# Performance work log

Measured on AMD Instinct MI355X. Metric: run time of the kernel, lower is better.

## Reference

```python
import jax, jax.numpy as jnp
import numpy as np

D_MODEL = 256
NHEAD = 8
D_FF = 2 * D_MODEL
N_LAYERS = 4
LAYER_NAMES = ("self", "cross", "self", "cross")
EPS_ATTN = 1e-6
EPS_LN = 1e-5


def pos_encoding(x):
    # LoFTR-style 2D sinusoidal positional encoding, x: [N, C, H, W]
    n, c, h, w = x.shape
    d4 = c // 4
    # exp(arange(0, c//2, 2) * (-log(1e4) / (c//2)))
    div = jnp.exp(jnp.arange(d4, dtype=jnp.float32) * 2.0 * (-np.log(10000.0) / (c // 2)))
    xs = jnp.arange(w, dtype=jnp.float32)[None, None, :]   # [1,1,W]
    ys = jnp.arange(h, dtype=jnp.float32)[None, :, None]   # [1,H,1]
    dv = div[:, None, None]                                 # [d4,1,1]
    sx = jnp.broadcast_to(jnp.sin(xs * dv), (d4, h, w))
    cx = jnp.broadcast_to(jnp.cos(xs * dv), (d4, h, w))
    sy = jnp.broadcast_to(jnp.sin(ys * dv), (d4, h, w))
    cy = jnp.broadcast_to(jnp.cos(ys * dv), (d4, h, w))
    pe = jnp.stack([sx, cx, sy, cy], axis=1).reshape(c, h, w)  # channel order pe[0::4]=sin_x,...
    return x + pe[None]


def linear_attention(q, k, v):
    # q: [N,L,H,d], k/v: [N,S,H,d]
    Q = jax.nn.elu(q) + 1.0
    K = jax.nn.elu(k) + 1.0
    KV = jnp.einsum('nshd,nshm->nhmd', K, v)                 # [N,H,d,d]
    Z = 1.0 / (jnp.einsum('nlhd,nhd->nlh', Q, K.sum(axis=1)) + EPS_ATTN)
    return jnp.einsum('nlhd,nhmd,nlh->nlhm', Q, KV, Z)       # [N,L,H,d]


def layer_norm(x, g, b):
    m = jnp.mean(x, axis=-1, keepdims=True)
    v = jnp.mean(jnp.square(x - m), axis=-1, keepdims=True)
    return (x - m) / jnp.sqrt(v + EPS_LN) * g + b


def encoder_layer(x, src, p):
    N, L, _ = x.shape
    q = (x @ p['Wq'] + p['bq']).reshape(N, L, NHEAD, -1)
    S = src.shape[1]
    k = (src @ p['Wk'] + p['bk']).reshape(N, S, NHEAD, -1)
    v = (src @ p['Wv'] + p['bv']).reshape(N, S, NHEAD, -1)
    attn = linear_attention(q, k, v).reshape(N, L, -1) @ p['Wo'] + p['bo']
    x = layer_norm(x + attn, p['g1'], p['be1'])
    y = jax.nn.relu(x @ p['W1'] + p['b1']) @ p['W2'] + p['b2']
    return layer_norm(x + y, p['g2'], p['be2'])


def _params_at(i, Wq, bq, Wk, bk, Wv, bv, Wo, bo, W1, b1, W2, b2, g1, be1, g2, be2):
    return dict(Wq=Wq[i], bq=bq[i], Wk=Wk[i], bk=bk[i], Wv=Wv[i], bv=bv[i],
                Wo=Wo[i], bo=bo[i], W1=W1[i], b1=b1[i], W2=W2[i], b2=b2[i],
                g1=g1[i], be1=be1[i], g2=g2[i], be2=be2[i])


def setup_inputs() -> dict:
    key = jax.random.key(0)
    ks = jax.random.split(key, 16)
    N, C, H, W = 4, D_MODEL, 64, 64
    d, dff, Ln = D_MODEL, D_FF, N_LAYERS
    s = 1.0 / np.sqrt(d)
    sf = 1.0 / np.sqrt(dff)
    return {
        'ref_feature': jax.random.normal(ks[0], (N, C, H, W), jnp.float32),
        'src_feature': jax.random.normal(ks[1], (N, C, H, W), jnp.float32),
        'Wq': jax.random.normal(ks[2], (Ln, d, d), jnp.float32) * s,
        'bq': jnp.zeros((Ln, d), jnp.float32),
        'Wk': jax.random.normal(ks[3], (Ln, d, d), jnp.float32) * s,
        'bk': jnp.zeros((Ln, d), jnp.float32),
        'Wv': jax.random.normal(ks[4], (Ln, d, d), jnp.float32) * s,
        'bv': jnp.zeros((Ln, d), jnp.float32),
        'Wo': jax.random.normal(ks[5], (Ln, d, d), jnp.float32) * s,
        'bo': jnp.zeros((Ln, d), jnp.float32),
        'W1': jax.random.normal(ks[6], (Ln, d, dff), jnp.float32) * s,
        'b1': jnp.zeros((Ln, dff), jnp.float32),
        'W2': jax.random.normal(ks[7], (Ln, dff, d), jnp.float32) * sf,
        'b2': jnp.zeros((Ln, d), jnp.float32),
        'g1': jnp.ones((Ln, d), jnp.float32),
        'be1': jnp.zeros((Ln, d), jnp.float32),
        'g2': jnp.ones((Ln, d), jnp.float32),
        'be2': jnp.zeros((Ln, d), jnp.float32),
    }


def reference(ref_feature, src_feature, Wq, bq, Wk, bk, Wv, bv, Wo, bo,
              W1, b1, W2, b2, g1, be1, g2, be2):
    # FMT.forward(feat='cross')
    N, C, H, W = ref_feature.shape
    f0 = pos_encoding(ref_feature).transpose(0, 2, 3, 1).reshape(N, H * W, C)
    f1 = pos_encoding(src_feature).transpose(0, 2, 3, 1).reshape(N, H * W, C)
    p1 = jnp.concatenate([f0, f1], axis=0)   # [2N, L, C]
    p2 = jnp.concatenate([f1, f0], axis=0)
    for i, name in enumerate(LAYER_NAMES):
        p = _params_at(i, Wq, bq, Wk, bk, Wv, bv, Wo, bo, W1, b1, W2, b2, g1, be1, g2, be2)
        src = p1 if name == 'self' else p2
        p1 = encoder_layer(p1, src, p)
    out = p1.reshape(2 * N, H, W, C).transpose(0, 3, 1, 2)  # [2N, C, H, W]
    return out
```

## Files before the change

### kernel.cpp

```cpp
#include <hip/hip_runtime.h>
#include <hip/hip_bf16.h>

typedef __bf16 bf16;
typedef __attribute__((ext_vector_type(8))) __bf16 bf16x8;
typedef __attribute__((ext_vector_type(4))) __bf16 bf16x4;
typedef __attribute__((ext_vector_type(4))) float f32x4;

__device__ __forceinline__ bf16 f2bf(float f) { return (bf16)f; }

__device__ __forceinline__ void async_cp16(const void* g, void* l) {
    __builtin_amdgcn_global_load_lds(
        (const __attribute__((address_space(1))) unsigned int*)g,
        (__attribute__((address_space(3))) unsigned int*)l, 16, 0, 0);
}

__device__ __forceinline__ float pe_val(int c, int t) {
    int h = t >> 6, w = t & 63;
    int i = c >> 2, j = c & 3;
    float div = expf(-0.14391156831212787f * (float)i);
    float arg = ((j < 2) ? (float)w : (float)h) * div;
    return (j & 1) ? cosf(arg) : sinf(arg);
}

__global__ __launch_bounds__(1024) void encode_kernel(const float* __restrict__ ref,
                                                      const float* __restrict__ src,
                                                      bf16* __restrict__ Xb,
                                                      bf16* __restrict__ P2b) {
    __shared__ float tile[32][33];
    int n = blockIdx.z >> 1, sel = blockIdx.z & 1;
    const float* f = sel ? src : ref;
    int t = blockIdx.x * 32 + threadIdx.x;
    int c = blockIdx.y * 32 + threadIdx.y;
    float v = f[((size_t)n * 256 + c) * 4096 + t] + pe_val(c, t);
    tile[threadIdx.y][threadIdx.x] = v;
    __syncthreads();
    int tt = blockIdx.x * 32 + threadIdx.y;
    int cc = blockIdx.y * 32 + threadIdx.x;
    float o = tile[threadIdx.x][threadIdx.y];
    int bx = sel ? 4 + n : n;
    int bp = sel ? n : 4 + n;
    Xb [((size_t)bx * 4096 + tt) * 256 + cc] = f2bf(o);
    P2b[((size_t)bp * 4096 + tt) * 256 + cc] = f2bf(o);
}

__global__ __launch_bounds__(1024) void wt_conv(const float* __restrict__ Wq, const float* __restrict__ Wk,
                                                const float* __restrict__ Wv, const float* __restrict__ Wo,
                                                const float* __restrict__ W1, const float* __restrict__ W2,
                                                bf16* __restrict__ Wt) {
    __shared__ float t[32][33];
    int z = blockIdx.z, L = z / 6, m = z - L * 6;
    const float* src; int K, N, doff;
    if      (m == 0) { src = Wq + L * 65536;  K = 256; N = 256; doff = 0; }
    else if (m == 1) { src = Wk + L * 65536;  K = 256; N = 256; doff = 65536; }
    else if (m == 2) { src = Wv + L * 65536;  K = 256; N = 256; doff = 131072; }
    else if (m == 3) { src = Wo + L * 65536;  K = 256; N = 256; doff = 196608; }
    else if (m == 4) { src = W1 + L * 131072; K = 256; N = 512; doff = 262144; }
    else             { src = W2 + L * 131072; K = 512; N = 256; doff = 393216; }
    int n0 = blockIdx.x * 32, k0 = blockIdx.y * 32;
    if (n0 >= N || k0 >= K) return;
    t[threadIdx.y][threadIdx.x] = src[(size_t)(k0 + threadIdx.y) * N + n0 + threadIdx.x];
    __syncthreads();
    bf16* dst = Wt + (size_t)L * 524288 + doff;
    dst[(size_t)(n0 + threadIdx.y) * K + k0 + threadIdx.x] = f2bf(t[threadIdx.x][threadIdx.y]);
}

__global__ __launch_bounds__(256) void gemm_qkv(const bf16* __restrict__ Aq,
                                                const bf16* __restrict__ Akv,
                                                const bf16* __restrict__ Wt,
                                                const float* __restrict__ bq,
                                                const float* __restrict__ bk,
                                                const float* __restrict__ bv,
                                                bf16* __restrict__ Q,
                                                bf16* __restrict__ Ko,
                                                bf16* __restrict__ V) {
    __shared__ bf16 Als[128 * 64];
    __shared__ bf16 Bls[128 * 64];
    int tid = threadIdx.x;
    int wave = tid >> 6, lane = tid & 63;
    int bm = blockIdx.y * 128, bn = blockIdx.x * 128;
    int wm = (wave >> 1) * 64, wn = (wave & 1) * 64;
    int l15 = lane & 15, g = lane >> 4;
    const int K = 256;

    int seg = bn >> 8, cloc = bn & 255;
    const bf16* A = seg == 0 ? Aq : Akv;
    const float* bias = seg == 0 ? bq : (seg == 1 ? bk : bv);
    bf16* Out = seg == 0 ? Q : (seg == 1 ? Ko : V);
    bool do_elu = seg < 2;

    f32x4 acc[4][4] = {};

    for (int k0 = 0; k0 < K; k0 += 64) {
#pragma unroll
        for (int r = 0; r < 4; ++r) {
            int Lc = r * 256 + tid;
            int row = Lc >> 3, cs = Lc & 7;
            int gc = cs ^ (row & 7);
            async_cp16(A  + (size_t)(bm + row) * K + k0 + gc * 8, &Als[Lc * 8]);
            async_cp16(Wt + (size_t)(bn + row) * K + k0 + gc * 8, &Bls[Lc * 8]);
        }
        __syncthreads();
#pragma unroll
        for (int ks = 0; ks < 2; ++ks) {
            bf16x8 af[4], bfr[4];
#pragma unroll
            for (int i = 0; i < 4; ++i) {
                int row = wm + i * 16 + l15;
                int c = ks * 4 + g;
                af[i] = *(bf16x8*)&Als[row * 64 + ((c ^ (row & 7)) * 8)];
            }
#pragma unroll
            for (int j = 0; j < 4; ++j) {
                int row = wn + j * 16 + l15;
                int c = ks * 4 + g;
                bfr[j] = *(bf16x8*)&Bls[row * 64 + ((c ^ (row & 7)) * 8)];
            }
#pragma unroll
            for (int i = 0; i < 4; ++i)
#pragma unroll
                for (int j = 0; j < 4; ++j)
                    acc[i][j] = __builtin_amdgcn_mfma_f32_16x16x32_bf16(af[i], bfr[j], acc[i][j], 0, 0, 0);
        }
        __syncthreads();
    }

    int r4 = (lane >> 4) * 4;
#pragma unroll
    for (int i = 0; i < 4; ++i) {
#pragma unroll
        for (int j = 0; j < 4; ++j) {
            int cj = cloc + wn + j * 16 + l15;
            float bvv = bias[cj];
#pragma unroll
            for (int r = 0; r < 4; ++r) {
                int row = bm + wm + i * 16 + r4 + r;
                float v = acc[i][j][r] + bvv;
                if (do_elu) v = v > 0.f ? v + 1.f : expf(v);
                Out[(size_t)row * 256 + cj] = f2bf(v);
            }
        }
    }
}

template <int RELU>
__global__ __launch_bounds__(256) void gemm_mfma(const bf16* __restrict__ A,
                                                 const bf16* __restrict__ Wt,
                                                 const float* __restrict__ bias,
                                                 bf16* __restrict__ C,
                                                 int N, int K) {
    __shared__ bf16 Als[128 * 64];
    __shared__ bf16 Bls[128 * 64];
    int tid = threadIdx.x;
    int wave = tid >> 6, lane = tid & 63;
    int bm = blockIdx.y * 128, bn = blockIdx.x * 128;
    int wm = (wave >> 1) * 64, wn = (wave & 1) * 64;
    int l15 = lane & 15, g = lane >> 4;

    f32x4 acc[4][4] = {};

    for (int k0 = 0; k0 < K; k0 += 64) {
#pragma unroll
        for (int r = 0; r < 4; ++r) {
            int Lc = r * 256 + tid;
            int row = Lc >> 3, cs = Lc & 7;
            int gc = cs ^ (row & 7);
            async_cp16(A  + (size_t)(bm + row) * K + k0 + gc * 8, &Als[Lc * 8]);
            async_cp16(Wt + (size_t)(bn + row) * K + k0 + gc * 8, &Bls[Lc * 8]);
        }
        __syncthreads();
#pragma unroll
        for (int ks = 0; ks < 2; ++ks) {
            bf16x8 af[4], bfr[4];
#pragma unroll
            for (int i = 0; i < 4; ++i) {
                int row = wm + i * 16 + l15;
                int c = ks * 4 + g;
                af[i] = *(bf16x8*)&Als[row * 64 + ((c ^ (row & 7)) * 8)];
            }
#pragma unroll
            for (int j = 0; j < 4; ++j) {
                int row = wn + j * 16 + l15;
                int c = ks * 4 + g;
                bfr[j] = *(bf16x8*)&Bls[row * 64 + ((c ^ (row & 7)) * 8)];
            }
#pragma unroll
            for (int i = 0; i < 4; ++i)
#pragma unroll
                for (int j = 0; j < 4; ++j)
                    acc[i][j] = __builtin_amdgcn_mfma_f32_16x16x32_bf16(af[i], bfr[j], acc[i][j], 0, 0, 0);
        }
        __syncthreads();
    }

    int r4 = (lane >> 4) * 4;
#pragma unroll
    for (int i = 0; i < 4; ++i) {
#pragma unroll
        for (int j = 0; j < 4; ++j) {
            int col = bn + wn + j * 16 + l15;
            float bvv = bias[col];
#pragma unroll
            for (int r = 0; r < 4; ++r) {
                int row = bm + wm + i * 16 + r4 + r;
                float v = acc[i][j][r] + bvv;
                if (RELU) v = fmaxf(v, 0.f);
                C[(size_t)row * N + col] = f2bf(v);
            }
        }
    }
}

__global__ __launch_bounds__(256) void kv_prep_part(const bf16* __restrict__ Kb,
                                                    const bf16* __restrict__ Vb,
                                                    float* __restrict__ Pkv,
                                                    float* __restrict__ Pks) {
    __shared__ float Ks[128][32];
    __shared__ float Vs[128][32];
    int sp = blockIdx.x;
    int nh = blockIdx.y;
    int n = nh >> 3, h = nh & 7;
    int tid = threadIdx.x;
    int wave = tid >> 6, lane = tid & 63;
    int mg = lane >> 3;
    int dg = lane & 7;
    size_t base = ((size_t)n * 4096 + sp * 128) * 256 + h * 32;

#pragma unroll
    for (int p = 0; p < 2; ++p) {
        int r = p * 64 + (tid >> 2);
        int c = (tid & 3) * 8;
        bf16x8 k8 = *(const bf16x8*)(Kb + base + (size_t)r * 256 + c);
        bf16x8 v8 = *(const bf16x8*)(Vb + base + (size_t)r * 256 + c);
#pragma unroll
        for (int u = 0; u < 8; ++u) { Ks[r][c + u] = (float)k8[u]; Vs[r][c + u] = (float)v8[u]; }
    }
    __syncthreads();

    float acc[4][4] = {};
    float ks4[4] = {};
    int s0 = wave * 32;
    for (int s = s0; s < s0 + 32; ++s) {
        float4 kq = *(float4*)&Ks[s][dg * 4];
        float4 vq = *(float4*)&Vs[s][mg * 4];
        ks4[0] += kq.x; ks4[1] += kq.y; ks4[2] += kq.z; ks4[3] += kq.w;
        acc[0][0] += vq.x * kq.x; acc[0][1] += vq.x * kq.y; acc[0][2] += vq.x * kq.z; acc[0][3] += vq.x * kq.w;
        acc[1][0] += vq.y * kq.x; acc[1][1] += vq.y * kq.y; acc[1][2] += vq.y * kq.z; acc[1][3] += vq.y * kq.w;
        acc[2][0] += vq.z * kq.x; acc[2][1] += vq.z * kq.y; acc[2][2] += vq.z * kq.z; acc[2][3] += vq.z * kq.w;
        acc[3][0] += vq.w * kq.x; acc[3][1] += vq.w * kq.y; acc[3][2] += vq.w * kq.z; acc[3][3] += vq.w * kq.w;
    }
    __syncthreads();

    float* R  = &Ks[0][0];
    float* RS = &Vs[0][0];
#pragma unroll
    for (int mi = 0; mi < 4; ++mi)
#pragma unroll
        for (int dj = 0; dj < 4; ++dj)
            R[wave * 1024 + (mg * 4 + mi) * 32 + dg * 4 + dj] = acc[mi][dj];
    if (mg == 0)
#pragma unroll
        for (int dj = 0; dj < 4; ++dj) RS[wave * 32 + dg * 4 + dj] = ks4[dj];
    __syncthreads();

    int e = tid * 4;
    float4 o0 = *(float4*)&R[e];
    float4 o1 = *(float4*)&R[1024 + e];
    float4 o2 = *(float4*)&R[2048 + e];
    float4 o3 = *(float4*)&R[3072 + e];
    float4 o = make_float4(o0.x + o1.x + o2.x + o3.x, o0.y + o1.y + o2.y + o3.y,
                           o0.z + o1.z + o2.z + o3.z, o0.w + o1.w + o2.w + o3.w);
    *(float4*)&Pkv[((size_t)nh * 32 + sp) * 1024 + e] = o;
    if (tid < 32)
        Pks[((size_t)nh * 32 + sp) * 32 + tid] = RS[tid] + RS[32 + tid] + RS[64 + tid] + RS[96 + tid];
}

__global__ __launch_bounds__(256) void kv_reduce(const float* __restrict__ Pkv,
                                                 const float* __restrict__ Pks,
                                                 float* __restrict__ KV,
                                                 float* __restrict__ Ksum) {
    int nh = blockIdx.x;
    int e = threadIdx.x * 4;
    float4 s = make_float4(0.f, 0.f, 0.f, 0.f);
    for (int sp = 0; sp < 32; ++sp) {
        float4 p = *(const float4*)&Pkv[((size_t)nh * 32 + sp) * 1024 + e];
        s.x += p.x; s.y += p.y; s.z += p.z; s.w += p.w;
    }
    *(float4*)&KV[(size_t)nh * 1024 + e] = s;
    if (threadIdx.x < 32) {
        float ss = 0.f;
        for (int sp = 0; sp < 32; ++sp) ss += Pks[((size_t)nh * 32 + sp) * 32 + threadIdx.x];
        Ksum[nh * 32 + threadIdx.x] = ss;
    }
}

__global__ __launch_bounds__(256) void attn_apply(const bf16* __restrict__ Qb,
                                                  const float* __restrict__ KV,
                                                  const float* __restrict__ Ksum,
                                                  bf16* __restrict__ B) {
    __shared__ float Qs[32][260];
    __shared__ float Zs[32][8];
    int bx = blockIdx.x;
    int n = bx >> 7;
    int tok0 = (bx & 127) << 5;
    int tid = threadIdx.x;

    const bf16* qsrc = Qb + ((size_t)(n * 4096 + tok0)) * 256;
#pragma unroll
    for (int kk = 0; kk < 4; ++kk) {
        int e8 = tid + kk * 256;
        bf16x8 v = *(const bf16x8*)(qsrc + (size_t)e8 * 8);
        int t = e8 >> 5, c8 = e8 & 31;
#pragma unroll
        for (int u = 0; u < 8; ++u) Qs[t][c8 * 8 + u] = (float)v[u];
    }

    int h = tid >> 5, m = tid & 31;
    float kvr[32];
    const float* kvp = KV + (size_t)(n * 8 + h) * 1024 + m * 32;
#pragma unroll
    for (int c = 0; c < 8; ++c) *(float4*)&kvr[c * 4] = *(const float4*)(kvp + c * 4);
    __syncthreads();

    {
        int tz = tid >> 3, hz = tid & 7;
        const float* ksp = Ksum + n * 256 + hz * 32;
        float z = 0.f;
#pragma unroll
        for (int c = 0; c < 8; ++c) {
            float4 q = *(float4*)&Qs[tz][hz * 32 + c * 4];
            float4 k = *(const float4*)(ksp + c * 4);
            z += q.x * k.x + q.y * k.y + q.z * k.z + q.w * k.w;
        }
        Zs[tz][hz] = 1.f / (z + 1e-6f);
    }
    __syncthreads();

    bf16* outp = B + ((size_t)(n * 4096 + tok0)) * 256 + tid;
#pragma unroll 2
    for (int t = 0; t < 32; ++t) {
        float acc = 0.f;
#pragma unroll
        for (int c = 0; c < 8; ++c) {
            float4 q = *(float4*)&Qs[t][h * 32 + c * 4];
            acc += q.x * kvr[c * 4 + 0] + q.y * kvr[c * 4 + 1]
                 + q.z * kvr[c * 4 + 2] + q.w * kvr[c * 4 + 3];
        }
        outp[(size_t)t * 256] = f2bf(acc * Zs[t][h]);
    }
}

__global__ __launch_bounds__(256) void ln_res(bf16* __restrict__ Xb,
                                              const bf16* __restrict__ G,
                                              const float* __restrict__ g,
                                              const float* __restrict__ b) {
    int row = blockIdx.x * 4 + (threadIdx.x >> 6);
    int lane = threadIdx.x & 63;
    int c = lane * 4;
    bf16x4 xb = *(const bf16x4*)(Xb + (size_t)row * 256 + c);
    bf16x4 gb = *(const bf16x4*)(G + (size_t)row * 256 + c);
    float4 v;
    v.x = (float)xb[0] + (float)gb[0];
    v.y = (float)xb[1] + (float)gb[1];
    v.z = (float)xb[2] + (float)gb[2];
    v.w = (float)xb[3] + (float)gb[3];
    float s  = v.x + v.y + v.z + v.w;
    float sq = v.x * v.x + v.y * v.y + v.z * v.z + v.w * v.w;
#pragma unroll
    for (int off = 32; off > 0; off >>= 1) {
        s  += __shfl_xor(s,  off);
        sq += __shfl_xor(sq, off);
    }
    float mean = s * (1.f / 256.f);
    float var  = sq * (1.f / 256.f) - mean * mean;
    float rstd = rsqrtf(var + 1e-5f);
    float4 o;
    o.x = (v.x - mean) * rstd * g[c + 0] + b[c + 0];
    o.y = (v.y - mean) * rstd * g[c + 1] + b[c + 1];
    o.z = (v.z - mean) * rstd * g[c + 2] + b[c + 2];
    o.w = (v.w - mean) * rstd * g[c + 3] + b[c + 3];
    bf16x4 ob; ob[0] = f2bf(o.x); ob[1] = f2bf(o.y); ob[2] = f2bf(o.z); ob[3] = f2bf(o.w);
    *(bf16x4*)(Xb + (size_t)row * 256 + c) = ob;
}

__global__ __launch_bounds__(1024) void store_kernel(const bf16* __restrict__ Xb,
                                                     float* __restrict__ out) {
    __shared__ float tile[32][33];
    int b = blockIdx.z;
    int t0 = blockIdx.x * 32, c0 = blockIdx.y * 32;
    tile[threadIdx.y][threadIdx.x] =
        (float)Xb[((size_t)b * 4096 + t0 + threadIdx.y) * 256 + c0 + threadIdx.x];
    __syncthreads();
    out[((size_t)b * 256 + c0 + threadIdx.y) * 4096 + t0 + threadIdx.x] =
        tile[threadIdx.x][threadIdx.y];
}

extern "C" void kernel_launch(void* const* d_in, const int* in_sizes, int n_in,
                              void* d_out, int out_size, void* d_ws, size_t ws_size,
                              hipStream_t stream) {
    const float* ref  = (const float*)d_in[0];
    const float* srcf = (const float*)d_in[1];
    const float* Wq = (const float*)d_in[2];
    const float* bq = (const float*)d_in[3];
    const float* Wk = (const float*)d_in[4];
    const float* bk = (const float*)d_in[5];
    const float* Wv = (const float*)d_in[6];
    const float* bv = (const float*)d_in[7];
    const float* Wo = (const float*)d_in[8];
    const float* bo = (const float*)d_in[9];
    const float* W1 = (const float*)d_in[10];
    const float* b1 = (const float*)d_in[11];
    const float* W2 = (const float*)d_in[12];
    const float* b2 = (const float*)d_in[13];
    const float* g1 = (const float*)d_in[14];
    const float* be1 = (const float*)d_in[15];
    const float* g2 = (const float*)d_in[16];
    const float* be2 = (const float*)d_in[17];

    const size_t SZ = (size_t)8 * 4096 * 256;
    float* ws  = (float*)d_ws;
    float* KVb = ws;
    float* Ksb = KVb + 65536;
    float* Pkv = Ksb + 2048;
    float* Pks = Pkv + 2097152;
    bf16*  Wt  = (bf16*)(Pks + 65536);
    bf16*  Xb  = Wt + 2097152;
    bf16*  P2b = Xb + SZ;
    bf16*  Qb  = P2b + SZ;
    bf16*  Kb  = (bf16*)d_out;
    bf16*  Vb  = Kb + SZ;
    bf16*  Bb  = Kb;
    bf16*  Hb  = Kb;

    wt_conv<<<dim3(16, 16, 24), dim3(32, 32), 0, stream>>>(Wq, Wk, Wv, Wo, W1, W2, Wt);
    encode_kernel<<<dim3(128, 8, 8), dim3(32, 32), 0, stream>>>(ref, srcf, Xb, P2b);

    for (int L = 0; L < 4; ++L) {
        const bf16* WtL = Wt + (size_t)L * 524288;
        const bf16* Akv = (L & 1) ? P2b : Xb;
        gemm_qkv<<<dim3(6, 256), 256, 0, stream>>>(Xb, Akv, WtL,
                                                   bq + L * 256, bk + L * 256, bv + L * 256,
                                                   Qb, Kb, Vb);
        kv_prep_part<<<dim3(32, 64), 256, 0, stream>>>(Kb, Vb, Pkv, Pks);
        kv_reduce<<<64, 256, 0, stream>>>(Pkv, Pks, KVb, Ksb);
        attn_apply<<<1024, 256, 0, stream>>>(Qb, KVb, Ksb, Bb);
        gemm_mfma<0><<<dim3(2, 256), 256, 0, stream>>>(Bb, WtL + 196608, bo + L * 256, Qb, 256, 256);
        ln_res<<<8192, 256, 0, stream>>>(Xb, Qb, g1 + L * 256, be1 + L * 256);
        gemm_mfma<1><<<dim3(4, 256), 256, 0, stream>>>(Xb, WtL + 262144, b1 + L * 512, Hb, 512, 256);
        gemm_mfma<0><<<dim3(2, 256), 256, 0, stream>>>(Hb, WtL + 393216, b2 + L * 256, Qb, 256, 512);
        ln_res<<<8192, 256, 0, stream>>>(Xb, Qb, g2 + L * 256, be2 + L * 256);
    }

    store_kernel<<<dim3(128, 8, 8), dim3(32, 32), 0, stream>>>(Xb, (float*)d_out);
}
```

Baseline: 729.5 us.

## Fuse output-projection and FFN2 GEMMs with residual LayerNorm epilogue

Adds a gemm_ln kernel in which each 512-thread block computes a full 128x256 output tile, stages it in LDS, then applies bias, residual add and LayerNorm before writing Xb. This replaces the separate GEMM plus ln_res pair for both LayerNorms, removing the intermediate Qb round trip and two launches per layer. kv_reduce is also split across 4 blocks per head to spread the reduction over more CUs. The fused kernel launches only 256 blocks with a single-stage K loop and no prefetch, so load latency may be less well hidden than in the original GEMM.

```diff
diff --git a/kernel.cpp b/kernel.cpp
--- a/kernel.cpp
+++ b/kernel.cpp
@@ -210,6 +210,112 @@
     }
 }
 
+__global__ __launch_bounds__(512) void gemm_ln(const bf16* __restrict__ A,
+                                               const bf16* __restrict__ Wt,
+                                               const float* __restrict__ bias,
+                                               bf16* __restrict__ Xb,
+                                               const float* __restrict__ g,
+                                               const float* __restrict__ b,
+                                               int K) {
+    __shared__ __align__(16) char smem[128 * 260 * 2];
+    bf16* Als = (bf16*)smem;
+    bf16* Bls = (bf16*)(smem + 16384);
+    bf16* Cls = (bf16*)smem;
+
+    int tid = threadIdx.x;
+    int wave = tid >> 6, lane = tid & 63;
+    int bm = blockIdx.x * 128;
+    int wm = (wave >> 2) * 64, wn = (wave & 3) * 64;
+    int l15 = lane & 15, gg = lane >> 4;
+
+    f32x4 acc[4][4] = {};
+
+    for (int k0 = 0; k0 < K; k0 += 64) {
+#pragma unroll
+        for (int r = 0; r < 2; ++r) {
+            int Lc = r * 512 + tid;
+            int row = Lc >> 3, cs = Lc & 7;
+            int gc = cs ^ (row & 7);
+            async_cp16(A + (size_t)(bm + row) * K + k0 + gc * 8, &Als[Lc * 8]);
+        }
+#pragma unroll
+        for (int r = 0; r < 4; ++r) {
+            int Lc = r * 512 + tid;
+            int row = Lc >> 3, cs = Lc & 7;
+            int gc = cs ^ (row & 7);
+            async_cp16(Wt + (size_t)row * K + k0 + gc * 8, &Bls[Lc * 8]);
+        }
+        __syncthreads();
+#pragma unroll
+        for (int ks = 0; ks < 2; ++ks) {
+            bf16x8 af[4], bfr[4];
+#pragma unroll
+            for (int i = 0; i < 4; ++i) {
+                int row = wm + i * 16 + l15;
+                int c = ks * 4 + gg;
+                af[i] = *(bf16x8*)&Als[row * 64 + ((c ^ (row & 7)) * 8)];
+            }
+#pragma unroll
+            for (int j = 0; j < 4; ++j) {
+                int row = wn + j * 16 + l15;
+                int c = ks * 4 + gg;
+                bfr[j] = *(bf16x8*)&Bls[row * 64 + ((c ^ (row & 7)) * 8)];
+            }
+#pragma unroll
+            for (int i = 0; i < 4; ++i)
+#pragma unroll
+                for (int j = 0; j < 4; ++j)
+                    acc[i][j] = __builtin_amdgcn_mfma_f32_16x16x32_bf16(af[i], bfr[j], acc[i][j], 0, 0, 0);
+        }
+        __syncthreads();
+    }
+
+    int r4 = (lane >> 4) * 4;
+#pragma unroll
+    for (int j = 0; j < 4; ++j) {
+        int col = wn + j * 16 + l15;
+        float bvv = bias[col];
+#pragma unroll
+        for (int i = 0; i < 4; ++i)
+#pragma unroll
+            for (int r = 0; r < 4; ++r)
+                Cls[(wm + i * 16 + r4 + r) * 260 + col] = f2bf(acc[i][j][r] + bvv);
+    }
+    __syncthreads();
+
+    int c4 = lane * 4;
+    float4 gw = *(const float4*)&g[c4];
+    float4 bw = *(const float4*)&b[c4];
+#pragma unroll 2
+    for (int rw = 0; rw < 16; ++rw) {
+        int row = wave * 16 + rw;
+        size_t gidx = (size_t)(bm + row) * 256 + c4;
+        bf16x4 xb = *(const bf16x4*)(Xb + gidx);
+        bf16x4 cb = *(const bf16x4*)&Cls[row * 260 + c4];
+        float4 v;
+        v.x = (float)xb[0] + (float)cb[0];
+        v.y = (float)xb[1] + (float)cb[1];
+        v.z = (float)xb[2] + (float)cb[2];
+        v.w = (float)xb[3] + (float)cb[3];
+        float s  = v.x + v.y + v.z + v.w;
+        float sq = v.x * v.x + v.y * v.y + v.z * v.z + v.w * v.w;
+#pragma unroll
+        for (int off = 32; off > 0; off >>= 1) {
+            s  += __shfl_xor(s,  off);
+            sq += __shfl_xor(sq, off);
+        }
+        float mean = s * (1.f / 256.f);
+        float var  = sq * (1.f / 256.f) - mean * mean;
+        float rstd = rsqrtf(var + 1e-5f);
+        bf16x4 ob;
+        ob[0] = f2bf((v.x - mean) * rstd * gw.x + bw.x);
+        ob[1] = f2bf((v.y - mean) * rstd * gw.y + bw.y);
+        ob[2] = f2bf((v.z - mean) * rstd * gw.z + bw.z);
+        ob[3] = f2bf((v.w - mean) * rstd * gw.w + bw.w);
+        *(bf16x4*)(Xb + gidx) = ob;
+    }
+}
+
 __global__ __launch_bounds__(256) void kv_prep_part(const bf16* __restrict__ Kb,
                                                     const bf16* __restrict__ Vb,
                                                     float* __restrict__ Pkv,
@@ -274,19 +380,20 @@
         Pks[((size_t)nh * 32 + sp) * 32 + tid] = RS[tid] + RS[32 + tid] + RS[64 + tid] + RS[96 + tid];
 }
 
-__global__ __launch_bounds__(256) void kv_reduce(const float* __restrict__ Pkv,
-                                                 const float* __restrict__ Pks,
-                                                 float* __restrict__ KV,
-                                                 float* __restrict__ Ksum) {
+__global__ __launch_bounds__(64) void kv_reduce(const float* __restrict__ Pkv,
+                                                const float* __restrict__ Pks,
+                                                float* __restrict__ KV,
+                                                float* __restrict__ Ksum) {
     int nh = blockIdx.x;
-    int e = threadIdx.x * 4;
+    int q = blockIdx.y;
+    int e = (q * 64 + threadIdx.x) * 4;
     float4 s = make_float4(0.f, 0.f, 0.f, 0.f);
     for (int sp = 0; sp < 32; ++sp) {
         float4 p = *(const float4*)&Pkv[((size_t)nh * 32 + sp) * 1024 + e];
         s.x += p.x; s.y += p.y; s.z += p.z; s.w += p.w;
     }
     *(float4*)&KV[(size_t)nh * 1024 + e] = s;
-    if (threadIdx.x < 32) {
+    if (q == 0 && threadIdx.x < 32) {
         float ss = 0.f;
         for (int sp = 0; sp < 32; ++sp) ss += Pks[((size_t)nh * 32 + sp) * 32 + threadIdx.x];
         Ksum[nh * 32 + threadIdx.x] = ss;
@@ -347,39 +454,6 @@
         }
         outp[(size_t)t * 256] = f2bf(acc * Zs[t][h]);
     }
-}
-
-__global__ __launch_bounds__(256) void ln_res(bf16* __restrict__ Xb,
-                                              const bf16* __restrict__ G,
-                                              const float* __restrict__ g,
-                                              const float* __restrict__ b) {
-    int row = blockIdx.x * 4 + (threadIdx.x >> 6);
-    int lane = threadIdx.x & 63;
-    int c = lane * 4;
-    bf16x4 xb = *(const bf16x4*)(Xb + (size_t)row * 256 + c);
-    bf16x4 gb = *(const bf16x4*)(G + (size_t)row * 256 + c);
-    float4 v;
-    v.x = (float)xb[0] + (float)gb[0];
-    v.y = (float)xb[1] + (float)gb[1];
-    v.z = (float)xb[2] + (float)gb[2];
-    v.w = (float)xb[3] + (float)gb[3];
-    float s  = v.x + v.y + v.z + v.w;
-    float sq = v.x * v.x + v.y * v.y + v.z * v.z + v.w * v.w;
-#pragma unroll
-    for (int off = 32; off > 0; off >>= 1) {
-        s  += __shfl_xor(s,  off);
-        sq += __shfl_xor(sq, off);
-    }
-    float mean = s * (1.f / 256.f);
-    float var  = sq * (1.f / 256.f) - mean * mean;
-    float rstd = rsqrtf(var + 1e-5f);
-    float4 o;
-    o.x = (v.x - mean) * rstd * g[c + 0] + b[c + 0];
-    o.y = (v.y - mean) * rstd * g[c + 1] + b[c + 1];
-    o.z = (v.z - mean) * rstd * g[c + 2] + b[c + 2];
-    o.w = (v.w - mean) * rstd * g[c + 3] + b[c + 3];
-    bf16x4 ob; ob[0] = f2bf(o.x); ob[1] = f2bf(o.y); ob[2] = f2bf(o.z); ob[3] = f2bf(o.w);
-    *(bf16x4*)(Xb + (size_t)row * 256 + c) = ob;
 }
 
 __global__ __launch_bounds__(1024) void store_kernel(const bf16* __restrict__ Xb,
@@ -441,13 +515,13 @@
                                                    bq + L * 256, bk + L * 256, bv + L * 256,
                                                    Qb, Kb, Vb);
         kv_prep_part<<<dim3(32, 64), 256, 0, stream>>>(Kb, Vb, Pkv, Pks);
-        kv_reduce<<<64, 256, 0, stream>>>(Pkv, Pks, KVb, Ksb);
+        kv_reduce<<<dim3(64, 4), 64, 0, stream>>>(Pkv, Pks, KVb, Ksb);
         attn_apply<<<1024, 256, 0, stream>>>(Qb, KVb, Ksb, Bb);
-        gemm_mfma<0><<<dim3(2, 256), 256, 0, stream>>>(Bb, WtL + 196608, bo + L * 256, Qb, 256, 256);
-        ln_res<<<8192, 256, 0, stream>>>(Xb, Qb, g1 + L * 256, be1 + L * 256);
+        gemm_ln<<<256, 512, 0, stream>>>(Bb, WtL + 196608, bo + L * 256, Xb,
+                                         g1 + L * 256, be1 + L * 256, 256);
         gemm_mfma<1><<<dim3(4, 256), 256, 0, stream>>>(Xb, WtL + 262144, b1 + L * 512, Hb, 512, 256);
-        gemm_mfma<0><<<dim3(2, 256), 256, 0, stream>>>(Hb, WtL + 393216, b2 + L * 256, Qb, 256, 512);
-        ln_res<<<8192, 256, 0, stream>>>(Xb, Qb, g2 + L * 256, be2 + L * 256);
+        gemm_ln<<<256, 512, 0, stream>>>(Hb, WtL + 393216, b2 + L * 256, Xb,
+                                         g2 + L * 256, be2 + L * 256, 512);
     }
 
     store_kernel<<<dim3(128, 8, 8), dim3(32, 32), 0, stream>>>(Xb, (float*)d_out);
```

Result: faster. 691.0 us (-5.3%).
